# Kernel tuning notes

Measured on AMD Instinct MI355X. Metric: run time of the kernel, lower is better.

The kernel has to match this reference:

```python
import jax, jax.numpy as jnp
import numpy as np

# ---- instant-NGP / torch-ngp style 2D hash-grid constants (from __init__ config) ----
NUM_LEVELS = 16
LEVEL_DIM = 2
BASE_RES = 16
MAX_PARAMS = 2 ** 19  # log2_hashmap_size = 19
PER_LEVEL_SCALE = float(np.exp2(np.log2(2048.0 / 16.0) / (NUM_LEVELS - 1)))  # desired_resolution overrides per_level_scale
PRIME_Y = np.uint32(2654435761)
DIVIDE_FACTOR = 1.0
FEAT_DIM = NUM_LEVELS * LEVEL_DIM  # 32
MAX_LEVELS = 12  # set_level_auto(500000)

def _meta():
    scales, sizes, offsets = [], [], [0]
    for l in range(NUM_LEVELS):
        scale = BASE_RES * PER_LEVEL_SCALE ** l - 1.0
        res = int(np.ceil(scale)) + 1
        params = min(MAX_PARAMS, res * res)
        params = int(np.ceil(params / 8) * 8)  # align to 8 like torch-ngp
        scales.append(scale)
        sizes.append((res, params))
        offsets.append(offsets[-1] + params)
    return scales, sizes, offsets

SCALES, SIZES, OFFSETS = _meta()
TOTAL_PARAMS = OFFSETS[-1]  # 2761312


def hash_grid_encode(x, table):
    """x: [N,2] in [0,1]; table: [TOTAL_PARAMS, LEVEL_DIM]. Returns [N, FEAT_DIM]."""
    feats = []
    for l in range(NUM_LEVELS):  # fixed small unroll over levels
        scale = SCALES[l]
        res, size = SIZES[l]
        off = OFFSETS[l]
        pos = x * scale + 0.5
        g0 = jnp.floor(pos)
        frac = pos - g0
        g0 = g0.astype(jnp.uint32)
        out = jnp.zeros((x.shape[0], LEVEL_DIM), x.dtype)
        for cx in (0, 1):  # bilinear corners
            wx = frac[:, 0] if cx else 1.0 - frac[:, 0]
            gx = g0[:, 0] + np.uint32(cx)
            for cy in (0, 1):
                wy = frac[:, 1] if cy else 1.0 - frac[:, 1]
                gy = g0[:, 1] + np.uint32(cy)
                if res * res <= size:  # dense (tiled) indexing at coarse levels
                    idx = (gx + gy * np.uint32(res)) % np.uint32(size)
                else:  # spatial hash at fine levels
                    idx = (gx ^ (gy * PRIME_Y)) % np.uint32(size)
                out = out + (wx * wy)[:, None] * table[off + idx.astype(jnp.int32)]
        feats.append(out)
    return jnp.concatenate(feats, axis=-1)


def setup_inputs() -> dict:
    key = jax.random.key(0)
    k1, k2, k3, k4 = jax.random.split(key, 4)
    N = 2_000_000
    init = lambda k: (jax.random.uniform(k, (TOTAL_PARAMS, LEVEL_DIM), jnp.float32) * 2.0 - 1.0) * 1e-4
    return {
        "input": jax.random.uniform(k1, (N, 3), jnp.float32),  # points in [0,1)
        "table_xy": init(k2),
        "table_yz": init(k3),
        "table_xz": init(k4),
        "step": 20000,
    }


def reference(input, table_xy, table_yz, table_xz, step):
    level = min(step // 1000 + 1, MAX_LEVELS)  # static python int -> static mask
    mask = (jnp.arange(FEAT_DIM) < 2 * level).astype(input.dtype)[None, :]
    x = input / DIVIDE_FACTOR
    xy = hash_grid_encode(x[:, (0, 1)], table_xy) * mask
    yz = hash_grid_encode(x[:, (1, 2)], table_yz) * mask
    xz = hash_grid_encode(x[:, (0, 2)], table_xz) * mask
    return xy + yz + xz
```

## Files before the change

### kernel.cpp

```cpp
#include <hip/hip_runtime.h>
#include <cmath>
#include <cstdint>

namespace {

constexpr int kLevels = 12;
constexpr unsigned kNB = 32768;
constexpr unsigned kTileCap = 512;

typedef float f32x4 __attribute__((ext_vector_type(4)));
typedef float f32x4u __attribute__((ext_vector_type(4), aligned(8)));

struct LevelMeta { float scale; unsigned res; unsigned size; unsigned off; };
struct Meta { LevelMeta lv[kLevels]; };

__device__ inline unsigned spread5(unsigned v) {
  v &= 31u;
  v = (v | (v << 8)) & 0x0000100Fu;
  v = (v | (v << 4)) & 0x000010C3u;
  v = (v | (v << 2)) & 0x00001249u;
  return v;
}

__device__ inline unsigned bucket_of(float x, float y, float z) {
  unsigned xi = (unsigned)fminf(fmaxf(x * 32.0f, 0.0f), 31.0f);
  unsigned yi = (unsigned)fminf(fmaxf(y * 32.0f, 0.0f), 31.0f);
  unsigned zi = (unsigned)fminf(fmaxf(z * 32.0f, 0.0f), 31.0f);
  return spread5(xi) | (spread5(yi) << 1) | (spread5(zi) << 2);
}

}


__global__ __launch_bounds__(256) void k_hist(const float* __restrict__ xyz,
                                              unsigned* __restrict__ counts, int n) {
  const int i = blockIdx.x * blockDim.x + threadIdx.x;
  if (i >= n) return;
  atomicAdd(&counts[bucket_of(xyz[3 * i], xyz[3 * i + 1], xyz[3 * i + 2])], 1u);
}

__global__ __launch_bounds__(1024) void k_scan(const unsigned* __restrict__ counts,
                                               unsigned* __restrict__ cursor) {
  __shared__ unsigned part[1024];
  const int t = threadIdx.x;
  const int base = t * 32;
  unsigned loc[32];
  unsigned run = 0;
#pragma unroll
  for (int j = 0; j < 32; ++j) { loc[j] = run; run += counts[base + j]; }
  part[t] = run;
  __syncthreads();
  for (int off = 1; off < 1024; off <<= 1) {
    unsigned v = (t >= off) ? part[t - off] : 0u;
    __syncthreads();
    part[t] += v;
    __syncthreads();
  }
  const unsigned ebase = part[t] - run;
#pragma unroll
  for (int j = 0; j < 32; ++j) cursor[base + j] = ebase + loc[j];
}

__global__ __launch_bounds__(256) void k_scatter(const float* __restrict__ xyz,
                                                 unsigned* __restrict__ cursor,
                                                 f32x4* __restrict__ sorted, int n) {
  const int i = blockIdx.x * blockDim.x + threadIdx.x;
  if (i >= n) return;
  const float x = xyz[3 * i], y = xyz[3 * i + 1], z = xyz[3 * i + 2];
  const unsigned pos = atomicAdd(&cursor[bucket_of(x, y, z)], 1u);
  f32x4 v;
  v.x = x; v.y = y; v.z = z; v.w = __uint_as_float((unsigned)i);
  sorted[pos] = v;
}


__global__ __launch_bounds__(256) void k_main_sorted(
    const f32x4* __restrict__ sorted,
    const float* __restrict__ txy,
    const float* __restrict__ tyz,
    const float* __restrict__ txz,
    const int* __restrict__ step_ptr,
    float* __restrict__ out,
    int n, Meta meta)
{
  __shared__ float stg[4 * 2080];
  __shared__ float2 tiles[4 * kTileCap];
  __shared__ unsigned idxs[256];

  const int tid = threadIdx.x;
  const int wid = tid >> 6;
  const int lane = tid & 63;
  const int g = blockIdx.x * 256 + tid;
  const bool valid = g < n;
  const f32x4 s = sorted[valid ? g : (n - 1)];
  const unsigned row = valid ? __float_as_uint(s.w) : 0xFFFFFFFFu;

  const int step = *step_ptr;
  int level = step / 1000 + 1;
  level = level > kLevels ? kLevels : level;

  float mnx = s.x, mxx = s.x, mny = s.y, mxy = s.y, mnz = s.z, mxz = s.z;
#pragma unroll
  for (int m = 1; m < 64; m <<= 1) {
    mnx = fminf(mnx, __shfl_xor(mnx, m)); mxx = fmaxf(mxx, __shfl_xor(mxx, m));
    mny = fminf(mny, __shfl_xor(mny, m)); mxy = fmaxf(mxy, __shfl_xor(mxy, m));
    mnz = fminf(mnz, __shfl_xor(mnz, m)); mxz = fmaxf(mxz, __shfl_xor(mxz, m));
  }

  float2* tile = &tiles[wid * kTileCap];
  float* wlds = stg + wid * 2080;

  {
    const f32x4 z = {0.0f, 0.0f, 0.0f, 0.0f};
    *reinterpret_cast<f32x4*>(wlds + 6 * 260 + lane * 4) = z;
    *reinterpret_cast<f32x4*>(wlds + 7 * 260 + lane * 4) = z;
  }

  for (int l = 0; l < kLevels; ++l) {
    const LevelMeta lm = meta.lv[l];
    float a0 = 0.0f, a1 = 0.0f;

    auto plane = [&](float c0, float c1, float lo0, float hi0, float lo1, float hi1,
                     const float* __restrict__ tabf) {
      const float2* __restrict__ tab = reinterpret_cast<const float2*>(tabf) + lm.off;

      const float posx = fmaf(c0, lm.scale, 0.5f);
      const float posy = fmaf(c1, lm.scale, 0.5f);
      const float g0x = floorf(posx);
      const float g0y = floorf(posy);
      const float fx = posx - g0x;
      const float fy = posy - g0y;
      const unsigned ix = (unsigned)g0x;
      const unsigned iy = (unsigned)g0y;

      const unsigned ix0 = (unsigned)floorf(fmaf(lo0, lm.scale, 0.5f));
      const unsigned ix1 = (unsigned)floorf(fmaf(hi0, lm.scale, 0.5f));
      const unsigned iy0 = (unsigned)floorf(fmaf(lo1, lm.scale, 0.5f));
      const unsigned iy1 = (unsigned)floorf(fmaf(hi1, lm.scale, 0.5f));
      const unsigned C = ix1 - ix0 + 2u;
      const unsigned R = iy1 - iy0 + 2u;
      const unsigned S = C | 1u;

      float2 q00, q01, q10, q11;
      if (C <= 64u && R * S <= kTileCap) {
        const unsigned kk = 32u - __builtin_clz(C - 1u);
        const unsigned rpi = 64u >> kk;
        const unsigned I = (R + rpi - 1u) >> (6u - kk);
        const unsigned rr = lane >> kk;
        const unsigned cc = lane & ((1u << kk) - 1u);

        float2 v0 = make_float2(0.0f, 0.0f);
        unsigned d0 = rr * S + cc;
        bool ok0 = (cc < C) & (rr < R);
        {
          unsigned gi = (iy0 + rr) * lm.res + ix0 + cc;
          if (gi >= lm.size) gi -= lm.size;
          if (ok0) v0 = tab[gi];
        }
        for (unsigned t = 1; t < I; ++t) {
          const unsigned r = t * rpi + rr;
          float2 v1 = make_float2(0.0f, 0.0f);
          const bool ok1 = (cc < C) & (r < R);
          unsigned gi = (iy0 + r) * lm.res + ix0 + cc;
          if (gi >= lm.size) gi -= lm.size;
          if (ok1) v1 = tab[gi];
          if (ok0) tile[d0] = v0;
          v0 = v1; d0 = r * S + cc; ok0 = ok1;
        }
        if (ok0) tile[d0] = v0;

        const unsigned a = (iy - iy0) * S + (ix - ix0);
        q00 = tile[a];
        q10 = tile[a + 1];
        q01 = tile[a + S];
        q11 = tile[a + S + 1];
      } else {
        unsigned i00 = ix + iy * lm.res;
        unsigned i01 = i00 + lm.res;
        if (i01 >= lm.size) i01 -= lm.size;
        const f32x4 r0 = *reinterpret_cast<const f32x4u*>(tab + i00);
        const f32x4 r1 = *reinterpret_cast<const f32x4u*>(tab + i01);
        const float2 tf = *tab;
        const bool w0 = (i00 == lm.size - 1u);
        const bool w1 = (i01 == lm.size - 1u);
        q00 = make_float2(r0.x, r0.y);
        q10 = w0 ? tf : make_float2(r0.z, r0.w);
        q01 = make_float2(r1.x, r1.y);
        q11 = w1 ? tf : make_float2(r1.z, r1.w);
      }

      const float w00 = (1.0f - fx) * (1.0f - fy);
      const float w01 = (1.0f - fx) * fy;
      const float w10 = fx * (1.0f - fy);
      const float w11 = fx * fy;
      a0 += w00 * q00.x + w01 * q01.x + w10 * q10.x + w11 * q11.x;
      a1 += w00 * q00.y + w01 * q01.y + w10 * q10.y + w11 * q11.y;
    };

    plane(s.x, s.y, mnx, mxx, mny, mxy, txy);
    plane(s.y, s.z, mny, mxy, mnz, mxz, tyz);
    plane(s.x, s.z, mnx, mxx, mnz, mxz, txz);

    float2 pr = (l < level) ? make_float2(a0, a1) : make_float2(0.0f, 0.0f);
    const int chunk = l >> 1;
    const int ofs = (l & 1) * 2;
    *reinterpret_cast<float2*>(wlds + chunk * 260 + lane * 4 + ofs) = pr;
  }

  idxs[tid] = row;
  __syncthreads();

#pragma unroll
  for (int q = 0; q < 8; ++q) {
    const int p = q * 8 + (lane >> 3);
    const int c = lane & 7;
    const unsigned r = idxs[wid * 64 + p];
    const f32x4 v = *reinterpret_cast<const f32x4*>(wlds + c * 260 + p * 4);
    if (r != 0xFFFFFFFFu)
      __builtin_nontemporal_store(v, reinterpret_cast<f32x4*>(out) + (size_t)r * 8 + c);
  }
}


__global__ __launch_bounds__(256) void k_fused_linear(
    const float* __restrict__ xyz,
    const float* __restrict__ txy,
    const float* __restrict__ tyz,
    const float* __restrict__ txz,
    const int* __restrict__ step_ptr,
    float* __restrict__ out,
    int n, Meta meta)
{
  __shared__ float lds[4 * 2048];
  const int tid = threadIdx.x;
  const int wid = tid >> 6;
  const int lane = tid & 63;
  const int bbase = blockIdx.x * 256;
  const int i = bbase + tid;
  const int pi = i < n ? i : (n - 1);

  const int step = *step_ptr;
  int level = step / 1000 + 1;
  level = level > kLevels ? kLevels : level;
  const int active = 2 * level;

  const float px = xyz[3 * pi], py = xyz[3 * pi + 1], pz = xyz[3 * pi + 2];
  float acc[2 * kLevels];
#pragma unroll
  for (int k = 0; k < 2 * kLevels; ++k) acc[k] = 0.0f;

  auto do_plane = [&](float c0, float c1, const float* __restrict__ tabf) {
    const float2* __restrict__ tab = reinterpret_cast<const float2*>(tabf);
#pragma unroll
    for (int l = 0; l < kLevels; ++l) {
      const LevelMeta lm = meta.lv[l];
      const float2* tb = tab + lm.off;
      const float posx = fmaf(c0, lm.scale, 0.5f);
      const float posy = fmaf(c1, lm.scale, 0.5f);
      const float g0x = floorf(posx), g0y = floorf(posy);
      const float fx = posx - g0x, fy = posy - g0y;
      const unsigned ix = (unsigned)g0x, iy = (unsigned)g0y;
      unsigned i00 = ix + iy * lm.res;
      unsigned i01 = i00 + lm.res;
      if (i01 >= lm.size) i01 -= lm.size;
      const f32x4 r0 = *reinterpret_cast<const f32x4u*>(tb + i00);
      const f32x4 r1 = *reinterpret_cast<const f32x4u*>(tb + i01);
      const float2 tf = *tb;
      const bool w0 = (i00 == lm.size - 1u), w1 = (i01 == lm.size - 1u);
      const float t10x = w0 ? tf.x : r0.z, t10y = w0 ? tf.y : r0.w;
      const float t11x = w1 ? tf.x : r1.z, t11y = w1 ? tf.y : r1.w;
      const float w00 = (1.0f - fx) * (1.0f - fy);
      const float w01 = (1.0f - fx) * fy;
      const float w10 = fx * (1.0f - fy);
      const float w11 = fx * fy;
      acc[2 * l + 0] += w00 * r0.x + w01 * r1.x + w10 * t10x + w11 * t11x;
      acc[2 * l + 1] += w00 * r0.y + w01 * r1.y + w10 * t10y + w11 * t11y;
    }
  };
  do_plane(px, py, txy);
  do_plane(py, pz, tyz);
  do_plane(px, pz, txz);

#pragma unroll
  for (int k = 0; k < 2 * kLevels; ++k)
    if (k >= active) acc[k] = 0.0f;

  float* wlds = lds + wid * 2048;
#pragma unroll
  for (int c = 0; c < 8; ++c) {
    f32x4 v;
    v.x = c < 6 ? acc[4 * c + 0] : 0.0f;
    v.y = c < 6 ? acc[4 * c + 1] : 0.0f;
    v.z = c < 6 ? acc[4 * c + 2] : 0.0f;
    v.w = c < 6 ? acc[4 * c + 3] : 0.0f;
    *reinterpret_cast<f32x4*>(wlds + c * 256 + lane * 4) = v;
  }
  __syncthreads();

  const long long wbase = (long long)bbase + wid * 64;
  f32x4* obase = reinterpret_cast<f32x4*>(out) + wbase * 8;
#pragma unroll
  for (int q = 0; q < 8; ++q) {
    const int p = q * 8 + (lane >> 3);
    const int c = lane & 7;
    const f32x4 v = *reinterpret_cast<const f32x4*>(wlds + c * 256 + p * 4);
    if (wbase + p < n)
      __builtin_nontemporal_store(v, obase + q * 64 + lane);
  }
}

extern "C" void kernel_launch(void* const* d_in, const int* in_sizes, int n_in,
                              void* d_out, int out_size, void* d_ws, size_t ws_size,
                              hipStream_t stream) {
  const float* xyz = (const float*)d_in[0];
  const float* txy = (const float*)d_in[1];
  const float* tyz = (const float*)d_in[2];
  const float* txz = (const float*)d_in[3];
  const int* step  = (const int*)d_in[4];
  float* out = (float*)d_out;
  const int n = in_sizes[0] / 3;

  Meta meta;
  unsigned off = 0;
  const double pls = std::exp2(std::log2(2048.0 / 16.0) / 15.0);
  for (int l = 0; l < 16; ++l) {
    const double scale = 16.0 * std::pow(pls, (double)l) - 1.0;
    const unsigned res = (unsigned)std::ceil(scale) + 1u;
    unsigned long long params = (unsigned long long)res * (unsigned long long)res;
    if (params > (1ull << 19)) params = (1ull << 19);
    params = ((params + 7ull) / 8ull) * 8ull;
    if (l < kLevels) {
      meta.lv[l].scale = (float)scale;
      meta.lv[l].res = res;
      meta.lv[l].size = (unsigned)params;
      meta.lv[l].off = off;
    }
    off += (unsigned)params;
  }

  const dim3 block(256);
  const dim3 grid((unsigned)((n + 255) / 256));

  const size_t sorted_off = 256 * 1024;
  const size_t need = sorted_off + (size_t)n * sizeof(f32x4);

  if (ws_size >= need) {
    unsigned* counts = (unsigned*)d_ws;
    unsigned* cursor = counts + kNB;
    f32x4* sorted = (f32x4*)((char*)d_ws + sorted_off);

    hipMemsetAsync(counts, 0, kNB * sizeof(unsigned), stream);
    hipLaunchKernelGGL(k_hist, grid, block, 0, stream, xyz, counts, n);
    hipLaunchKernelGGL(k_scan, dim3(1), dim3(1024), 0, stream, counts, cursor);
    hipLaunchKernelGGL(k_scatter, grid, block, 0, stream, xyz, cursor, sorted, n);
    hipLaunchKernelGGL(k_main_sorted, grid, block, 0, stream,
                       sorted, txy, tyz, txz, step, out, n, meta);
  } else {
    hipLaunchKernelGGL(k_fused_linear, grid, block, 0, stream,
                       xyz, txy, tyz, txz, step, out, n, meta);
  }
}
```

Baseline: 559.4 us.

## Software-pipeline table gathers two plane-levels ahead with register prefetch buffers

Restructures the per-level, per-plane loop of the sorted kernel into an ISSUE/CONSUME pipeline. Global table gathers for unit u+2 are issued into register buffers before unit u is written to a shared LDS arena and interpolated, so memory latency overlaps with compute. Tile parameters are made wave-uniform with readfirstlane. The tile and output staging buffers are merged into one per-wave LDS region, and the block-wide barrier is dropped. In exchange, register use grows (prefetch buffers plus per-level accumulators), which may lower occupancy, and the tiled path is now capped at eight row iterations.

```diff
diff --git a/kernel.cpp b/kernel.cpp
--- a/kernel.cpp
+++ b/kernel.cpp
@@ -6,7 +6,7 @@
 
 constexpr int kLevels = 12;
 constexpr unsigned kNB = 32768;
-constexpr unsigned kTileCap = 512;
+constexpr unsigned kCap = 520;
 
 typedef float f32x4 __attribute__((ext_vector_type(4)));
 typedef float f32x4u __attribute__((ext_vector_type(4), aligned(8)));
@@ -83,8 +83,7 @@
     float* __restrict__ out,
     int n, Meta meta)
 {
-  __shared__ float stg[4 * 2080];
-  __shared__ float2 tiles[4 * kTileCap];
+  __shared__ float smem[4][2080];
   __shared__ unsigned idxs[256];
 
   const int tid = threadIdx.x;
@@ -93,11 +92,12 @@
   const int g = blockIdx.x * 256 + tid;
   const bool valid = g < n;
   const f32x4 s = sorted[valid ? g : (n - 1)];
-  const unsigned row = valid ? __float_as_uint(s.w) : 0xFFFFFFFFu;
+  idxs[tid] = valid ? __float_as_uint(s.w) : 0xFFFFFFFFu;
 
   const int step = *step_ptr;
   int level = step / 1000 + 1;
   level = level > kLevels ? kLevels : level;
+  const int active = 2 * level;
 
   float mnx = s.x, mxx = s.x, mny = s.y, mxy = s.y, mnz = s.z, mxz = s.z;
 #pragma unroll
@@ -107,115 +107,156 @@
     mnz = fminf(mnz, __shfl_xor(mnz, m)); mxz = fmaxf(mxz, __shfl_xor(mxz, m));
   }
 
-  float2* tile = &tiles[wid * kTileCap];
-  float* wlds = stg + wid * 2080;
-
-  {
-    const f32x4 z = {0.0f, 0.0f, 0.0f, 0.0f};
-    *reinterpret_cast<f32x4*>(wlds + 6 * 260 + lane * 4) = z;
-    *reinterpret_cast<f32x4*>(wlds + 7 * 260 + lane * 4) = z;
-  }
-
-  for (int l = 0; l < kLevels; ++l) {
+  const float cA[3] = {s.x, s.y, s.x};
+  const float cB[3] = {s.y, s.z, s.z};
+  const float loA[3] = {mnx, mny, mnx}, hiA[3] = {mxx, mxy, mxx};
+  const float loB[3] = {mny, mnz, mnz}, hiB[3] = {mxy, mxz, mxz};
+  const float2* tabs[3] = {reinterpret_cast<const float2*>(txy),
+                           reinterpret_cast<const float2*>(tyz),
+                           reinterpret_cast<const float2*>(txz)};
+
+  float2* arena = reinterpret_cast<float2*>(&smem[wid][0]);
+
+  float acc[2 * kLevels];
+#pragma unroll
+  for (int k = 0; k < 2 * kLevels; ++k) acc[k] = 0.0f;
+
+  float2 pv[3][8];
+  unsigned pI[3], pkk[3], pS[3], pC[3], pR[3], pX0[3], pY0[3], pT[3];
+
+  auto ISSUE = [&](int u) {
+    const int l = u / 3, p = u % 3, b = u % 3;
     const LevelMeta lm = meta.lv[l];
-    float a0 = 0.0f, a1 = 0.0f;
-
-    auto plane = [&](float c0, float c1, float lo0, float hi0, float lo1, float hi1,
-                     const float* __restrict__ tabf) {
-      const float2* __restrict__ tab = reinterpret_cast<const float2*>(tabf) + lm.off;
-
-      const float posx = fmaf(c0, lm.scale, 0.5f);
-      const float posy = fmaf(c1, lm.scale, 0.5f);
-      const float g0x = floorf(posx);
-      const float g0y = floorf(posy);
-      const float fx = posx - g0x;
-      const float fy = posy - g0y;
-      const unsigned ix = (unsigned)g0x;
-      const unsigned iy = (unsigned)g0y;
-
-      const unsigned ix0 = (unsigned)floorf(fmaf(lo0, lm.scale, 0.5f));
-      const unsigned ix1 = (unsigned)floorf(fmaf(hi0, lm.scale, 0.5f));
-      const unsigned iy0 = (unsigned)floorf(fmaf(lo1, lm.scale, 0.5f));
-      const unsigned iy1 = (unsigned)floorf(fmaf(hi1, lm.scale, 0.5f));
-      const unsigned C = ix1 - ix0 + 2u;
-      const unsigned R = iy1 - iy0 + 2u;
-      const unsigned S = C | 1u;
-
-      float2 q00, q01, q10, q11;
-      if (C <= 64u && R * S <= kTileCap) {
-        const unsigned kk = 32u - __builtin_clz(C - 1u);
-        const unsigned rpi = 64u >> kk;
-        const unsigned I = (R + rpi - 1u) >> (6u - kk);
-        const unsigned rr = lane >> kk;
-        const unsigned cc = lane & ((1u << kk) - 1u);
-
-        float2 v0 = make_float2(0.0f, 0.0f);
-        unsigned d0 = rr * S + cc;
-        bool ok0 = (cc < C) & (rr < R);
-        {
-          unsigned gi = (iy0 + rr) * lm.res + ix0 + cc;
+    const float2* __restrict__ tab = tabs[p] + lm.off;
+
+    const unsigned tx0 = (unsigned)floorf(fmaf(loA[p], lm.scale, 0.5f));
+    const unsigned tx1 = (unsigned)floorf(fmaf(hiA[p], lm.scale, 0.5f));
+    const unsigned ty0 = (unsigned)floorf(fmaf(loB[p], lm.scale, 0.5f));
+    const unsigned ty1 = (unsigned)floorf(fmaf(hiB[p], lm.scale, 0.5f));
+    const unsigned C = tx1 - tx0 + 2u;
+    const unsigned R = ty1 - ty0 + 2u;
+    const unsigned kk0 = 32u - (unsigned)__builtin_clz(C - 1u);
+    const unsigned rpi0 = 64u >> (kk0 > 6u ? 6u : kk0);
+    const unsigned sI0 = (R + rpi0 - 1u) / rpi0;
+    const unsigned tiled =
+        (C <= 64u && R * (C | 1u) <= kCap && sI0 <= 8u) ? 1u : 0u;
+    const unsigned sT = (unsigned)__builtin_amdgcn_readfirstlane((int)tiled);
+    pT[b] = sT;
+
+    if (sT) {
+      const unsigned sC = (unsigned)__builtin_amdgcn_readfirstlane((int)C);
+      const unsigned sR = (unsigned)__builtin_amdgcn_readfirstlane((int)R);
+      const unsigned sX0 = (unsigned)__builtin_amdgcn_readfirstlane((int)tx0);
+      const unsigned sY0 = (unsigned)__builtin_amdgcn_readfirstlane((int)ty0);
+      const unsigned sI = (unsigned)__builtin_amdgcn_readfirstlane((int)sI0);
+      const unsigned kk = 32u - (unsigned)__builtin_clz(sC - 1u);
+      const unsigned rpi = 64u >> kk;
+      pC[b] = sC; pR[b] = sR; pS[b] = sC | 1u; pkk[b] = kk; pI[b] = sI;
+      pX0[b] = sX0; pY0[b] = sY0;
+      const unsigned rr = lane >> kk;
+      const unsigned cc = lane & ((1u << kk) - 1u);
+#pragma unroll
+      for (unsigned t = 0; t < 8; ++t) {
+        if (t < sI) {
+          unsigned gi = (sY0 + t * rpi + rr) * lm.res + sX0 + cc;
           if (gi >= lm.size) gi -= lm.size;
-          if (ok0) v0 = tab[gi];
+          pv[b][t] = tab[gi];
         }
-        for (unsigned t = 1; t < I; ++t) {
+      }
+    } else {
+      const float posx = fmaf(cA[p], lm.scale, 0.5f);
+      const float posy = fmaf(cB[p], lm.scale, 0.5f);
+      const unsigned ix = (unsigned)floorf(posx);
+      const unsigned iy = (unsigned)floorf(posy);
+      unsigned i00 = ix + iy * lm.res;
+      unsigned i01 = i00 + lm.res;
+      if (i01 >= lm.size) i01 -= lm.size;
+      const f32x4 r0 = *reinterpret_cast<const f32x4u*>(tab + i00);
+      const f32x4 r1 = *reinterpret_cast<const f32x4u*>(tab + i01);
+      pv[b][0] = make_float2(r0.x, r0.y);
+      pv[b][1] = make_float2(r0.z, r0.w);
+      pv[b][2] = make_float2(r1.x, r1.y);
+      pv[b][3] = make_float2(r1.z, r1.w);
+    }
+  };
+
+  auto CONSUME = [&](int u) {
+    const int l = u / 3, p = u % 3, b = u % 3;
+    const LevelMeta lm = meta.lv[l];
+    const float2* __restrict__ tab = tabs[p] + lm.off;
+
+    const float posx = fmaf(cA[p], lm.scale, 0.5f);
+    const float posy = fmaf(cB[p], lm.scale, 0.5f);
+    const float g0x = floorf(posx), g0y = floorf(posy);
+    const float fx = posx - g0x, fy = posy - g0y;
+    const unsigned ix = (unsigned)g0x, iy = (unsigned)g0y;
+
+    float2 q00, q01, q10, q11;
+    if (pT[b]) {
+      const unsigned kk = pkk[b], sS = pS[b], sI = pI[b];
+      const unsigned sC = pC[b], sR = pR[b];
+      const unsigned rpi = 64u >> kk;
+      const unsigned rr = lane >> kk;
+      const unsigned cc = lane & ((1u << kk) - 1u);
+#pragma unroll
+      for (unsigned t = 0; t < 8; ++t) {
+        if (t < sI) {
           const unsigned r = t * rpi + rr;
-          float2 v1 = make_float2(0.0f, 0.0f);
-          const bool ok1 = (cc < C) & (r < R);
-          unsigned gi = (iy0 + r) * lm.res + ix0 + cc;
-          if (gi >= lm.size) gi -= lm.size;
-          if (ok1) v1 = tab[gi];
-          if (ok0) tile[d0] = v0;
-          v0 = v1; d0 = r * S + cc; ok0 = ok1;
+          if ((cc < sC) & (r < sR)) arena[r * sS + cc] = pv[b][t];
         }
-        if (ok0) tile[d0] = v0;
-
-        const unsigned a = (iy - iy0) * S + (ix - ix0);
-        q00 = tile[a];
-        q10 = tile[a + 1];
-        q01 = tile[a + S];
-        q11 = tile[a + S + 1];
-      } else {
-        unsigned i00 = ix + iy * lm.res;
-        unsigned i01 = i00 + lm.res;
-        if (i01 >= lm.size) i01 -= lm.size;
-        const f32x4 r0 = *reinterpret_cast<const f32x4u*>(tab + i00);
-        const f32x4 r1 = *reinterpret_cast<const f32x4u*>(tab + i01);
-        const float2 tf = *tab;
-        const bool w0 = (i00 == lm.size - 1u);
-        const bool w1 = (i01 == lm.size - 1u);
-        q00 = make_float2(r0.x, r0.y);
-        q10 = w0 ? tf : make_float2(r0.z, r0.w);
-        q01 = make_float2(r1.x, r1.y);
-        q11 = w1 ? tf : make_float2(r1.z, r1.w);
       }
-
-      const float w00 = (1.0f - fx) * (1.0f - fy);
-      const float w01 = (1.0f - fx) * fy;
-      const float w10 = fx * (1.0f - fy);
-      const float w11 = fx * fy;
-      a0 += w00 * q00.x + w01 * q01.x + w10 * q10.x + w11 * q11.x;
-      a1 += w00 * q00.y + w01 * q01.y + w10 * q10.y + w11 * q11.y;
-    };
-
-    plane(s.x, s.y, mnx, mxx, mny, mxy, txy);
-    plane(s.y, s.z, mny, mxy, mnz, mxz, tyz);
-    plane(s.x, s.z, mnx, mxx, mnz, mxz, txz);
-
-    float2 pr = (l < level) ? make_float2(a0, a1) : make_float2(0.0f, 0.0f);
-    const int chunk = l >> 1;
-    const int ofs = (l & 1) * 2;
-    *reinterpret_cast<float2*>(wlds + chunk * 260 + lane * 4 + ofs) = pr;
-  }
-
-  idxs[tid] = row;
-  __syncthreads();
-
+      const unsigned a = (iy - pY0[b]) * sS + (ix - pX0[b]);
+      q00 = arena[a];
+      q10 = arena[a + 1];
+      q01 = arena[a + sS];
+      q11 = arena[a + sS + 1];
+    } else {
+      unsigned i00 = ix + iy * lm.res;
+      unsigned i01 = i00 + lm.res;
+      if (i01 >= lm.size) i01 -= lm.size;
+      const float2 tf = *tab;
+      q00 = pv[b][0];
+      q10 = (i00 == lm.size - 1u) ? tf : pv[b][1];
+      q01 = pv[b][2];
+      q11 = (i01 == lm.size - 1u) ? tf : pv[b][3];
+    }
+
+    const float w00 = (1.0f - fx) * (1.0f - fy);
+    const float w01 = (1.0f - fx) * fy;
+    const float w10 = fx * (1.0f - fy);
+    const float w11 = fx * fy;
+    acc[2 * l + 0] += w00 * q00.x + w01 * q01.x + w10 * q10.x + w11 * q11.x;
+    acc[2 * l + 1] += w00 * q00.y + w01 * q01.y + w10 * q10.y + w11 * q11.y;
+  };
+
+  ISSUE(0);
+  ISSUE(1);
+#pragma unroll
+  for (int u = 0; u < 36; ++u) {
+    if (u + 2 < 36) ISSUE(u + 2);
+    CONSUME(u);
+  }
+
+#pragma unroll
+  for (int k = 0; k < 2 * kLevels; ++k)
+    if (k >= active) acc[k] = 0.0f;
+
+  float* wlds = &smem[wid][0];
+#pragma unroll
+  for (int c = 0; c < 8; ++c) {
+    f32x4 v;
+    v.x = c < 6 ? acc[4 * c + 0] : 0.0f;
+    v.y = c < 6 ? acc[4 * c + 1] : 0.0f;
+    v.z = c < 6 ? acc[4 * c + 2] : 0.0f;
+    v.w = c < 6 ? acc[4 * c + 3] : 0.0f;
+    *reinterpret_cast<f32x4*>(wlds + c * 260 + lane * 4) = v;
+  }
 #pragma unroll
   for (int q = 0; q < 8; ++q) {
-    const int p = q * 8 + (lane >> 3);
+    const int p2 = q * 8 + (lane >> 3);
     const int c = lane & 7;
-    const unsigned r = idxs[wid * 64 + p];
-    const f32x4 v = *reinterpret_cast<const f32x4*>(wlds + c * 260 + p * 4);
+    const unsigned r = idxs[wid * 64 + p2];
+    const f32x4 v = *reinterpret_cast<const f32x4*>(wlds + c * 260 + p2 * 4);
     if (r != 0xFFFFFFFFu)
       __builtin_nontemporal_store(v, reinterpret_cast<f32x4*>(out) + (size_t)r * 8 + c);
   }
```

New measurement: 1.225 ms. 119% more time.
